# Kernel tuning notes

Measured on AMD Instinct MI355X. Metric: run time of the kernel, lower is better.

The kernel has to match this reference:

```python
import jax, jax.numpy as jnp
import numpy as np

N_NODES = 100000
N_EDGES = 1600000
NUM_GRAPHS = 128


def setup_inputs() -> dict:
    key = jax.random.key(0)
    k1, k2, k3, k4, k5, k6 = jax.random.split(key, 6)
    x = jax.random.normal(k1, (N_NODES, 69), dtype=jnp.float32)
    src = jax.random.randint(k2, (N_EDGES,), 0, N_NODES)
    dst = jax.random.randint(k3, (N_EDGES,), 0, N_NODES)
    graph_ids = jnp.sort(jax.random.randint(k4, (N_NODES,), 0, NUM_GRAPHS))
    # Glorot-uniform weights like dgl GraphConv (bias=False)
    lim1 = np.sqrt(6.0 / (69 + 128))
    lim2 = np.sqrt(6.0 / (128 + 64))
    W1 = jax.random.uniform(k5, (69, 128), minval=-lim1, maxval=lim1, dtype=jnp.float32)
    W2 = jax.random.uniform(k6, (128, 64), minval=-lim2, maxval=lim2, dtype=jnp.float32)
    return {"x": x, "W1": W1, "W2": W2, "src": src, "dst": dst, "graph_ids": graph_ids}


def _graph_conv(feat, W, src, dst, inv_sqrt_out, inv_sqrt_in, n_nodes):
    # dgl GraphConv norm='both': D_out^{-1/2} -> SpMM(A) -> D_in^{-1/2} -> W
    h = feat * inv_sqrt_out[:, None]
    agg = jax.ops.segment_sum(h[src], dst, num_segments=n_nodes)  # [N, d]
    agg = agg * inv_sqrt_in[:, None]
    return agg @ W


def reference(x, W1, W2, src, dst, graph_ids):
    n = x.shape[0]
    ones = jnp.ones((src.shape[0],), dtype=x.dtype)
    out_deg = jax.ops.segment_sum(ones, src, num_segments=n)
    in_deg = jax.ops.segment_sum(ones, dst, num_segments=n)
    inv_sqrt_out = jax.lax.rsqrt(jnp.clip(out_deg, 1.0, None))
    inv_sqrt_in = jax.lax.rsqrt(jnp.clip(in_deg, 1.0, None))

    h = _graph_conv(x, W1, src, dst, inv_sqrt_out, inv_sqrt_in, n)
    h = jax.nn.relu(h)
    h = _graph_conv(h, W2, src, dst, inv_sqrt_out, inv_sqrt_in, n)
    h = jax.nn.relu(h)
    # dgl.max_nodes: per-graph max readout -> [num_graphs, 64]
    readout = jax.ops.segment_max(h, graph_ids, num_segments=NUM_GRAPHS)
    return readout
```

## Files before the change

### kernel.cpp

```cpp
#include <hip/hip_runtime.h>

#define N_NODES 100000
#define N_EDGES 1600000
#define NUM_GRAPHS 128

#define BSH 10
#define NBUCK 98
#define NBLKP 500
#define EPB (N_EDGES / NBLKP)
#define SOFF (NBUCK * NBLKP)
#define NSCAN (2 * NBUCK * NBLKP)
#define SCAN_BS 1024
#define NBSC ((NSCAN + SCAN_BS - 1) / SCAN_BS)

__device__ __forceinline__ unsigned bf16pair(float a, float b) {
    unsigned ua = __float_as_uint(a), ub = __float_as_uint(b);
    ua = (ua + 0x7FFFu + ((ua >> 16) & 1u)) >> 16;
    ub = (ub + 0x7FFFu + ((ub >> 16) & 1u)) >> 16;
    return ua | (ub << 16);
}
__device__ __forceinline__ float bflo(unsigned u) { return __uint_as_float(u << 16); }
__device__ __forceinline__ float bfhi(unsigned u) { return __uint_as_float(u & 0xFFFF0000u); }

__global__ __launch_bounds__(256) void part_hist(const int* __restrict__ src,
                                                 const int* __restrict__ dst,
                                                 int* __restrict__ cnt) {
    __shared__ int hd[4 * NBUCK], hs[4 * NBUCK];
    int t = threadIdx.x;
    for (int i = t; i < 4 * NBUCK; i += 256) { hd[i] = 0; hs[i] = 0; }
    __syncthreads();
    int wid = t >> 6;
    int* hdw = hd + wid * NBUCK;
    int* hsw = hs + wid * NBUCK;
    int e0 = blockIdx.x * EPB;
    for (int j = 4 * t; j + 3 < EPB; j += 1024) {
        int4 s4 = *(const int4*)(src + e0 + j);
        int4 d4 = *(const int4*)(dst + e0 + j);
        atomicAdd(&hdw[d4.x >> BSH], 1); atomicAdd(&hdw[d4.y >> BSH], 1);
        atomicAdd(&hdw[d4.z >> BSH], 1); atomicAdd(&hdw[d4.w >> BSH], 1);
        atomicAdd(&hsw[s4.x >> BSH], 1); atomicAdd(&hsw[s4.y >> BSH], 1);
        atomicAdd(&hsw[s4.z >> BSH], 1); atomicAdd(&hsw[s4.w >> BSH], 1);
    }
    __syncthreads();
    int bk = blockIdx.x;
    for (int i = t; i < NBUCK; i += 256) {
        cnt[i * NBLKP + bk] = hd[i] + hd[NBUCK + i] + hd[2 * NBUCK + i] + hd[3 * NBUCK + i];
        cnt[SOFF + i * NBLKP + bk] = hs[i] + hs[NBUCK + i] + hs[2 * NBUCK + i] + hs[3 * NBUCK + i];
    }
}

__global__ __launch_bounds__(256) void scan1(const int* __restrict__ cnt, int* __restrict__ excl,
                                             int* __restrict__ blksum, int n) {
    __shared__ int tmp[256];
    int t = threadIdx.x;
    int idx0 = blockIdx.x * SCAN_BS + t * 4;
    int v[4];
#pragma unroll
    for (int k = 0; k < 4; ++k) { int i = idx0 + k; v[k] = (i < n) ? cnt[i] : 0; }
    int sum = v[0] + v[1] + v[2] + v[3];
    tmp[t] = sum;
    __syncthreads();
    for (int off = 1; off < 256; off <<= 1) {
        int y = (t >= off) ? tmp[t - off] : 0;
        __syncthreads();
        tmp[t] += y;
        __syncthreads();
    }
    int run = (t > 0) ? tmp[t - 1] : 0;
#pragma unroll
    for (int k = 0; k < 4; ++k) { int i = idx0 + k; if (i < n) excl[i] = run; run += v[k]; }
    if (t == 255) blksum[blockIdx.x] = tmp[255];
}

__global__ __launch_bounds__(256) void scan2(int* __restrict__ blksum, int nb) {
    __shared__ int tmp[256];
    int t = threadIdx.x;
    int C = (nb + 255) / 256;
    int base = t * C;
    int s = 0;
    for (int k = 0; k < C; ++k) { int i = base + k; if (i < nb) s += blksum[i]; }
    tmp[t] = s;
    __syncthreads();
    for (int off = 1; off < 256; off <<= 1) {
        int y = (t >= off) ? tmp[t - off] : 0;
        __syncthreads();
        tmp[t] += y;
        __syncthreads();
    }
    int run = (t > 0) ? tmp[t - 1] : 0;
    for (int k = 0; k < C; ++k) {
        int i = base + k;
        if (i < nb) { int v = blksum[i]; blksum[i] = run; run += v; }
    }
}

__global__ __launch_bounds__(256) void part_scatter(const int* __restrict__ src,
                                                    const int* __restrict__ dst,
                                                    const int* __restrict__ cnt,
                                                    const int* __restrict__ blk,
                                                    unsigned* __restrict__ pdst,
                                                    unsigned short* __restrict__ psrc) {
    __shared__ int cd[NBUCK], cs[NBUCK];
    int bk = blockIdx.x;
    int t = threadIdx.x;
    for (int i = t; i < NBUCK; i += 256) {
        int ii = i * NBLKP + bk;
        cd[i] = cnt[ii] + blk[ii >> 10];
        int jj = SOFF + i * NBLKP + bk;
        cs[i] = cnt[jj] + blk[jj >> 10] - N_EDGES;
    }
    __syncthreads();
    int e0 = bk * EPB;
    for (int j = 4 * t; j + 3 < EPB; j += 1024) {
        int4 s4 = *(const int4*)(src + e0 + j);
        int4 d4 = *(const int4*)(dst + e0 + j);
        int ss[4] = { s4.x, s4.y, s4.z, s4.w };
        int dd[4] = { d4.x, d4.y, d4.z, d4.w };
#pragma unroll
        for (int u = 0; u < 4; ++u) {
            int s = ss[u], d = dd[u];
            int pd = atomicAdd(&cd[d >> BSH], 1);
            pdst[pd] = (unsigned)s | ((unsigned)(d & 1023) << 17);
            int ps = atomicAdd(&cs[s >> BSH], 1);
            psrc[ps] = (unsigned short)(s & 1023);
        }
    }
}

__global__ __launch_bounds__(1024) void build_csr(const unsigned* __restrict__ pdst,
                                                  const int* __restrict__ cnt,
                                                  const int* __restrict__ blk,
                                                  int* __restrict__ ecol, int* __restrict__ row_start,
                                                  float* __restrict__ isqi, int nN) {
    __shared__ int lh[1024];
    __shared__ int lsc[1024];
    int bu = blockIdx.x;
    int i0 = bu * NBLKP;
    int b0 = cnt[i0] + blk[i0 >> 10];
    int b1;
    if (bu == NBUCK - 1) b1 = N_EDGES;
    else { int i1 = i0 + NBLKP; b1 = cnt[i1] + blk[i1 >> 10]; }
    int t = threadIdx.x;
    lh[t] = 0;
    __syncthreads();
    for (int j = b0 + t; j < b1; j += 1024)
        atomicAdd(&lh[pdst[j] >> 17], 1);
    __syncthreads();
    int myc = lh[t];
    lsc[t] = myc;
    __syncthreads();
    for (int off = 1; off < 1024; off <<= 1) {
        int y = (t >= off) ? lsc[t - off] : 0;
        __syncthreads();
        lsc[t] += y;
        __syncthreads();
    }
    int excl = lsc[t] - myc;
    int node = (bu << BSH) + t;
    if (node < nN) {
        row_start[node] = b0 + excl;
        isqi[node] = rsqrtf(fmaxf((float)myc, 1.0f));
    }
    __syncthreads();
    lh[t] = b0 + excl;
    __syncthreads();
    for (int j = b0 + t; j < b1; j += 1024) {
        unsigned w = pdst[j];
        int pos = atomicAdd(&lh[w >> 17], 1);
        ecol[pos] = (int)(w & 0x1FFFFu);
    }
}

__global__ __launch_bounds__(1024) void src_deg(const unsigned short* __restrict__ psrc,
                                                const int* __restrict__ cnt,
                                                const int* __restrict__ blk,
                                                float* __restrict__ isqo, int nN) {
    __shared__ int lh[1024];
    int bu = blockIdx.x;
    int i0 = SOFF + bu * NBLKP;
    int b0 = cnt[i0] + blk[i0 >> 10] - N_EDGES;
    int b1;
    if (bu == NBUCK - 1) b1 = N_EDGES;
    else { int i1 = i0 + NBLKP; b1 = cnt[i1] + blk[i1 >> 10] - N_EDGES; }
    int t = threadIdx.x;
    lh[t] = 0;
    __syncthreads();
    for (int j = b0 + t; j < b1; j += 1024)
        atomicAdd(&lh[psrc[j]], 1);
    __syncthreads();
    int node = (bu << BSH) + t;
    if (node < nN) isqo[node] = rsqrtf(fmaxf((float)lh[t], 1.0f));
}

__global__ void prescale_kernel(const float* __restrict__ x, const float* __restrict__ isqo,
                                unsigned* __restrict__ xsu, int nN) {
    int wave = (int)(((unsigned)blockIdx.x * blockDim.x + threadIdx.x) >> 6);
    int lane = threadIdx.x & 63;
    if (wave >= nN || lane >= 36) return;
    float s = isqo[wave];
    int c = 2 * lane;
    float a = (c < 69) ? x[(size_t)wave * 69 + c] * s : 0.0f;
    float b = (c + 1 < 69) ? x[(size_t)wave * 69 + c + 1] * s : 0.0f;
    xsu[(size_t)wave * 36 + lane] = bf16pair(a, b);
}

__global__ void gather1_kernel(const unsigned* __restrict__ feat, const int* __restrict__ ecol,
                               const int* __restrict__ row_start, const float* __restrict__ dscale,
                               float* __restrict__ agg, int nN, int nE) {
    int wave = (int)(((unsigned)blockIdx.x * blockDim.x + threadIdx.x) >> 6);
    int lane = threadIdx.x & 63;
    if (wave >= nN) return;
    int beg = row_start[wave];
    int end = (wave == nN - 1) ? nE : row_start[wave + 1];
    bool act = (lane < 36);
    float ax = 0.0f, ay = 0.0f;
    for (int j0 = beg; j0 < end; j0 += 64) {
        int ne = min(64, end - j0);
        int eidx = (lane < ne) ? ecol[j0 + lane] : 0;
        int k = 0;
        for (; k + 8 <= ne; k += 8) {
            unsigned v[8];
#pragma unroll
            for (int u = 0; u < 8; ++u) {
                int s = __shfl(eidx, k + u);
                v[u] = act ? feat[(size_t)s * 36 + lane] : 0u;
            }
#pragma unroll
            for (int u = 0; u < 8; ++u) { ax += bflo(v[u]); ay += bfhi(v[u]); }
        }
        for (; k + 2 <= ne; k += 2) {
            int s0 = __shfl(eidx, k), s1 = __shfl(eidx, k + 1);
            unsigned v0 = act ? feat[(size_t)s0 * 36 + lane] : 0u;
            unsigned v1 = act ? feat[(size_t)s1 * 36 + lane] : 0u;
            ax += bflo(v0) + bflo(v1); ay += bfhi(v0) + bfhi(v1);
        }
        for (; k < ne; ++k) {
            int s = __shfl(eidx, k);
            unsigned v = act ? feat[(size_t)s * 36 + lane] : 0u;
            ax += bflo(v); ay += bfhi(v);
        }
    }
    if (act) {
        float dsc = dscale[wave];
        ((float2*)(agg + (size_t)wave * 72))[lane] = make_float2(ax * dsc, ay * dsc);
    }
}

__global__ void gather2_kernel(const unsigned* __restrict__ feat, const int* __restrict__ ecol,
                               const int* __restrict__ row_start, const float* __restrict__ dscale,
                               float* __restrict__ agg, int nN, int nE) {
    int wave = (int)(((unsigned)blockIdx.x * blockDim.x + threadIdx.x) >> 6);
    int lane = threadIdx.x & 63;
    if (wave >= nN) return;
    int beg = row_start[wave];
    int end = (wave == nN - 1) ? nE : row_start[wave + 1];
    int half = lane >> 5;
    int c = lane & 31;
    float ax = 0.0f, ay = 0.0f;
    for (int j0 = beg; j0 < end; j0 += 64) {
        int ne = min(64, end - j0);
        int eidx = (lane < ne) ? ecol[j0 + lane] : 0;
        int k = 0;
        for (; k + 16 <= ne; k += 16) {
            unsigned v[8];
#pragma unroll
            for (int u = 0; u < 8; ++u) {
                int s = __shfl(eidx, k + 2 * u + half);
                v[u] = feat[(size_t)s * 32 + c];
            }
#pragma unroll
            for (int u = 0; u < 8; ++u) { ax += bflo(v[u]); ay += bfhi(v[u]); }
        }
        for (; k + 2 <= ne; k += 2) {
            int s = __shfl(eidx, k + half);
            unsigned v = feat[(size_t)s * 32 + c];
            ax += bflo(v); ay += bfhi(v);
        }
        if (k < ne) {
            int s = __shfl(eidx, k);
            if (half == 0) {
                unsigned v = feat[(size_t)s * 32 + c];
                ax += bflo(v); ay += bfhi(v);
            }
        }
    }
    ax += __shfl_xor(ax, 32);
    ay += __shfl_xor(ay, 32);
    if (half == 0) {
        float dsc = dscale[wave];
        ((float2*)(agg + (size_t)wave * 64))[c] = make_float2(ax * dsc, ay * dsc);
    }
}

template<int KP, int K, int NO, bool RELU, bool SCALE, bool BF16OUT>
__global__ __launch_bounds__(256) void node_gemm(const float* __restrict__ in,
                                                 const float* __restrict__ W,
                                                 const float* __restrict__ rowscale,
                                                 void* __restrict__ out, int nN) {
    constexpr int CG = NO / 8;
    constexpr int RT = 256 / CG;
    constexpr int ROWS = RT * 4;
    __shared__ float Wl[KP * NO];
    for (int i = threadIdx.x; i < KP * NO; i += 256)
        Wl[i] = (i < K * NO) ? W[i] : 0.0f;
    __syncthreads();

    int cg = threadIdx.x % CG;
    int rt = threadIdx.x / CG;
    int row0 = blockIdx.x * ROWS + rt * 4;
    int c0 = cg * 8;

    float4 accL[4] = {};
    float4 accH[4] = {};
    int rclamp[4];
#pragma unroll
    for (int r = 0; r < 4; ++r) rclamp[r] = min(row0 + r, nN - 1);

#pragma unroll 2
    for (int k4 = 0; k4 < KP / 4; ++k4) {
        float4 a[4];
#pragma unroll
        for (int r = 0; r < 4; ++r)
            a[r] = *(const float4*)(in + (size_t)rclamp[r] * KP + k4 * 4);
#pragma unroll
        for (int kk = 0; kk < 4; ++kk) {
            int k = k4 * 4 + kk;
            float4 wlo = *(const float4*)&Wl[k * NO + c0];
            float4 whi = *(const float4*)&Wl[k * NO + c0 + 4];
#pragma unroll
            for (int r = 0; r < 4; ++r) {
                float ar = (kk == 0) ? a[r].x : (kk == 1) ? a[r].y : (kk == 2) ? a[r].z : a[r].w;
                accL[r].x += ar * wlo.x; accL[r].y += ar * wlo.y;
                accL[r].z += ar * wlo.z; accL[r].w += ar * wlo.w;
                accH[r].x += ar * whi.x; accH[r].y += ar * whi.y;
                accH[r].z += ar * whi.z; accH[r].w += ar * whi.w;
            }
        }
    }

#pragma unroll
    for (int r = 0; r < 4; ++r) {
        int row = row0 + r;
        if (row < nN) {
            float4 lo = accL[r], hi = accH[r];
            if (SCALE) {
                float sc = rowscale[row];
                lo.x *= sc; lo.y *= sc; lo.z *= sc; lo.w *= sc;
                hi.x *= sc; hi.y *= sc; hi.z *= sc; hi.w *= sc;
            }
            if (RELU) {
                lo.x = fmaxf(lo.x, 0.f); lo.y = fmaxf(lo.y, 0.f);
                lo.z = fmaxf(lo.z, 0.f); lo.w = fmaxf(lo.w, 0.f);
                hi.x = fmaxf(hi.x, 0.f); hi.y = fmaxf(hi.y, 0.f);
                hi.z = fmaxf(hi.z, 0.f); hi.w = fmaxf(hi.w, 0.f);
            }
            if (BF16OUT) {
                unsigned* ob = (unsigned*)out;
                uint4 p;
                p.x = bf16pair(lo.x, lo.y); p.y = bf16pair(lo.z, lo.w);
                p.z = bf16pair(hi.x, hi.y); p.w = bf16pair(hi.z, hi.w);
                *(uint4*)(ob + (size_t)row * (NO / 2) + c0 / 2) = p;
            } else {
                float* of = (float*)out;
                *(float4*)(of + (size_t)row * NO + c0) = lo;
                *(float4*)(of + (size_t)row * NO + c0 + 4) = hi;
            }
        }
    }
}

__global__ void readout_kernel(const float* __restrict__ agg2, const int* __restrict__ gid,
                               unsigned* __restrict__ out, int nN) {
    const int NPW = 32;
    int wave = (int)(((unsigned)blockIdx.x * blockDim.x + threadIdx.x) >> 6);
    int lane = threadIdx.x & 63;
    int n0 = wave * NPW;
    if (n0 >= nN) return;
    int curg = gid[n0];
    float best = 0.0f;
    for (int i = 0; i < NPW; ++i) {
        int n = n0 + i;
        if (n >= nN) break;
        int g = gid[n];
        float v = fmaxf(agg2[(size_t)n * 64 + lane], 0.0f);
        if (g != curg) {
            atomicMax(&out[curg * 64 + lane], __float_as_uint(best));
            curg = g;
            best = v;
        } else {
            best = fmaxf(best, v);
        }
    }
    atomicMax(&out[curg * 64 + lane], __float_as_uint(best));
}

extern "C" void kernel_launch(void* const* d_in, const int* in_sizes, int n_in,
                              void* d_out, int out_size, void* d_ws, size_t ws_size,
                              hipStream_t stream) {
    const float* x   = (const float*)d_in[0];
    const float* W1  = (const float*)d_in[1];
    const float* W2  = (const float*)d_in[2];
    const int*   src = (const int*)d_in[3];
    const int*   dst = (const int*)d_in[4];
    const int*   gid = (const int*)d_in[5];

    char* w = (char*)d_ws;
    float* isqo    = (float*)w;                 w += N_NODES * 4;
    float* isqi    = (float*)w;                 w += N_NODES * 4;
    int* row_start = (int*)w;                   w += N_NODES * 4;
    int* ecol      = (int*)w;                   w += (size_t)N_EDGES * 4;
    int* cnt       = (int*)w;                   w += (size_t)NSCAN * 4;
    int* blksum    = (int*)w;                   w += 1024 * 4;
    float* bufA    = (float*)w;                 w += (size_t)N_NODES * 72 * 4;
    char* bufB     = w;
    unsigned* pdst       = (unsigned*)bufB;
    unsigned* xsu        = (unsigned*)bufB;
    unsigned short* psrc = (unsigned short*)(bufB + (size_t)N_NODES * 36 * 4);
    float* h1            = (float*)bufB;
    float* agg2          = (float*)bufB;

    hipMemsetAsync(d_out, 0, (size_t)out_size * sizeof(float), stream);

    part_hist<<<NBLKP, 256, 0, stream>>>(src, dst, cnt);
    scan1<<<NBSC, 256, 0, stream>>>(cnt, cnt, blksum, NSCAN);
    scan2<<<1, 256, 0, stream>>>(blksum, NBSC);
    part_scatter<<<NBLKP, 256, 0, stream>>>(src, dst, cnt, blksum, pdst, psrc);
    build_csr<<<NBUCK, 1024, 0, stream>>>(pdst, cnt, blksum, ecol, row_start, isqi, N_NODES);
    src_deg<<<NBUCK, 1024, 0, stream>>>(psrc, cnt, blksum, isqo, N_NODES);
    prescale_kernel<<<(N_NODES * 64 + 255) / 256, 256, 0, stream>>>(x, isqo, xsu, N_NODES);

    gather1_kernel<<<(N_NODES * 64 + 255) / 256, 256, 0, stream>>>(
        xsu, ecol, row_start, isqi, bufA, N_NODES, N_EDGES);
    node_gemm<72, 69, 128, true, false, false><<<(N_NODES + 63) / 64, 256, 0, stream>>>(
        bufA, W1, nullptr, h1, N_NODES);

    node_gemm<128, 128, 64, false, true, true><<<(N_NODES + 127) / 128, 256, 0, stream>>>(
        h1, W2, isqo, (void*)bufA, N_NODES);
    gather2_kernel<<<(N_NODES * 64 + 255) / 256, 256, 0, stream>>>(
        (const unsigned*)bufA, ecol, row_start, isqi, agg2, N_NODES, N_EDGES);

    readout_kernel<<<((N_NODES + 31) / 32 * 64 + 255) / 256, 256, 0, stream>>>(
        agg2, gid, (unsigned*)d_out, N_NODES);
}
```

Baseline: 276.9 us.

## Merge CSR/degree kernels, split gather1 rows into halves, store h1 as bf16

Three changes. First, build_csr and src_deg are fused into one launch of 2*NBUCK blocks so the two independent passes run concurrently. Second, the layer-1 features are split into a 32-word main array and a 4-word tail array, so gather1 can use both wave halves on alternate edges, as gather2 already does, instead of leaving 28 lanes idle. Third, the first GEMM writes h1 in bf16 and the second GEMM reads bf16, halving h1 traffic at some cost in precision.

```diff
diff --git a/kernel.cpp b/kernel.cpp
--- a/kernel.cpp
+++ b/kernel.cpp
@@ -127,73 +127,70 @@
     }
 }
 
-__global__ __launch_bounds__(1024) void build_csr(const unsigned* __restrict__ pdst,
-                                                  const int* __restrict__ cnt,
-                                                  const int* __restrict__ blk,
-                                                  int* __restrict__ ecol, int* __restrict__ row_start,
-                                                  float* __restrict__ isqi, int nN) {
+__global__ __launch_bounds__(1024) void phase_d(const unsigned* __restrict__ pdst,
+                                                const unsigned short* __restrict__ psrc,
+                                                const int* __restrict__ cnt,
+                                                const int* __restrict__ blk,
+                                                int* __restrict__ ecol, int* __restrict__ row_start,
+                                                float* __restrict__ isqi, float* __restrict__ isqo,
+                                                int nN) {
     __shared__ int lh[1024];
     __shared__ int lsc[1024];
-    int bu = blockIdx.x;
-    int i0 = bu * NBLKP;
-    int b0 = cnt[i0] + blk[i0 >> 10];
-    int b1;
-    if (bu == NBUCK - 1) b1 = N_EDGES;
-    else { int i1 = i0 + NBLKP; b1 = cnt[i1] + blk[i1 >> 10]; }
     int t = threadIdx.x;
-    lh[t] = 0;
-    __syncthreads();
-    for (int j = b0 + t; j < b1; j += 1024)
-        atomicAdd(&lh[pdst[j] >> 17], 1);
-    __syncthreads();
-    int myc = lh[t];
-    lsc[t] = myc;
-    __syncthreads();
-    for (int off = 1; off < 1024; off <<= 1) {
-        int y = (t >= off) ? lsc[t - off] : 0;
-        __syncthreads();
-        lsc[t] += y;
-        __syncthreads();
-    }
-    int excl = lsc[t] - myc;
-    int node = (bu << BSH) + t;
-    if (node < nN) {
-        row_start[node] = b0 + excl;
-        isqi[node] = rsqrtf(fmaxf((float)myc, 1.0f));
-    }
-    __syncthreads();
-    lh[t] = b0 + excl;
-    __syncthreads();
-    for (int j = b0 + t; j < b1; j += 1024) {
-        unsigned w = pdst[j];
-        int pos = atomicAdd(&lh[w >> 17], 1);
-        ecol[pos] = (int)(w & 0x1FFFFu);
-    }
-}
-
-__global__ __launch_bounds__(1024) void src_deg(const unsigned short* __restrict__ psrc,
-                                                const int* __restrict__ cnt,
-                                                const int* __restrict__ blk,
-                                                float* __restrict__ isqo, int nN) {
-    __shared__ int lh[1024];
-    int bu = blockIdx.x;
-    int i0 = SOFF + bu * NBLKP;
-    int b0 = cnt[i0] + blk[i0 >> 10] - N_EDGES;
-    int b1;
-    if (bu == NBUCK - 1) b1 = N_EDGES;
-    else { int i1 = i0 + NBLKP; b1 = cnt[i1] + blk[i1 >> 10] - N_EDGES; }
-    int t = threadIdx.x;
-    lh[t] = 0;
-    __syncthreads();
-    for (int j = b0 + t; j < b1; j += 1024)
-        atomicAdd(&lh[psrc[j]], 1);
-    __syncthreads();
-    int node = (bu << BSH) + t;
-    if (node < nN) isqo[node] = rsqrtf(fmaxf((float)lh[t], 1.0f));
+    if (blockIdx.x < NBUCK) {
+        int bu = blockIdx.x;
+        int i0 = bu * NBLKP;
+        int b0 = cnt[i0] + blk[i0 >> 10];
+        int b1;
+        if (bu == NBUCK - 1) b1 = N_EDGES;
+        else { int i1 = i0 + NBLKP; b1 = cnt[i1] + blk[i1 >> 10]; }
+        lh[t] = 0;
+        __syncthreads();
+        for (int j = b0 + t; j < b1; j += 1024)
+            atomicAdd(&lh[pdst[j] >> 17], 1);
+        __syncthreads();
+        int myc = lh[t];
+        lsc[t] = myc;
+        __syncthreads();
+        for (int off = 1; off < 1024; off <<= 1) {
+            int y = (t >= off) ? lsc[t - off] : 0;
+            __syncthreads();
+            lsc[t] += y;
+            __syncthreads();
+        }
+        int excl = lsc[t] - myc;
+        int node = (bu << BSH) + t;
+        if (node < nN) {
+            row_start[node] = b0 + excl;
+            isqi[node] = rsqrtf(fmaxf((float)myc, 1.0f));
+        }
+        __syncthreads();
+        lh[t] = b0 + excl;
+        __syncthreads();
+        for (int j = b0 + t; j < b1; j += 1024) {
+            unsigned w = pdst[j];
+            int pos = atomicAdd(&lh[w >> 17], 1);
+            ecol[pos] = (int)(w & 0x1FFFFu);
+        }
+    } else {
+        int bu = blockIdx.x - NBUCK;
+        int i0 = SOFF + bu * NBLKP;
+        int b0 = cnt[i0] + blk[i0 >> 10] - N_EDGES;
+        int b1;
+        if (bu == NBUCK - 1) b1 = N_EDGES;
+        else { int i1 = i0 + NBLKP; b1 = cnt[i1] + blk[i1 >> 10] - N_EDGES; }
+        lh[t] = 0;
+        __syncthreads();
+        for (int j = b0 + t; j < b1; j += 1024)
+            atomicAdd(&lh[psrc[j]], 1);
+        __syncthreads();
+        int node = (bu << BSH) + t;
+        if (node < nN) isqo[node] = rsqrtf(fmaxf((float)lh[t], 1.0f));
+    }
 }
 
 __global__ void prescale_kernel(const float* __restrict__ x, const float* __restrict__ isqo,
-                                unsigned* __restrict__ xsu, int nN) {
+                                unsigned* __restrict__ xmain, unsigned* __restrict__ xtail, int nN) {
     int wave = (int)(((unsigned)blockIdx.x * blockDim.x + threadIdx.x) >> 6);
     int lane = threadIdx.x & 63;
     if (wave >= nN || lane >= 36) return;
@@ -201,48 +198,64 @@
     int c = 2 * lane;
     float a = (c < 69) ? x[(size_t)wave * 69 + c] * s : 0.0f;
     float b = (c + 1 < 69) ? x[(size_t)wave * 69 + c + 1] * s : 0.0f;
-    xsu[(size_t)wave * 36 + lane] = bf16pair(a, b);
-}
-
-__global__ void gather1_kernel(const unsigned* __restrict__ feat, const int* __restrict__ ecol,
-                               const int* __restrict__ row_start, const float* __restrict__ dscale,
-                               float* __restrict__ agg, int nN, int nE) {
+    unsigned p = bf16pair(a, b);
+    if (lane < 32) xmain[(size_t)wave * 32 + lane] = p;
+    else           xtail[(size_t)wave * 4 + (lane - 32)] = p;
+}
+
+__global__ void gather1_kernel(const unsigned* __restrict__ xmain, const unsigned* __restrict__ xtail,
+                               const int* __restrict__ ecol, const int* __restrict__ row_start,
+                               const float* __restrict__ dscale, float* __restrict__ agg,
+                               int nN, int nE) {
     int wave = (int)(((unsigned)blockIdx.x * blockDim.x + threadIdx.x) >> 6);
     int lane = threadIdx.x & 63;
     if (wave >= nN) return;
     int beg = row_start[wave];
     int end = (wave == nN - 1) ? nE : row_start[wave + 1];
-    bool act = (lane < 36);
-    float ax = 0.0f, ay = 0.0f;
+    int half = lane >> 5;
+    int c = lane & 31;
+    bool tact = (c < 4);
+    float ax = 0.0f, ay = 0.0f, tx = 0.0f, ty = 0.0f;
     for (int j0 = beg; j0 < end; j0 += 64) {
         int ne = min(64, end - j0);
         int eidx = (lane < ne) ? ecol[j0 + lane] : 0;
         int k = 0;
-        for (; k + 8 <= ne; k += 8) {
-            unsigned v[8];
+        for (; k + 16 <= ne; k += 16) {
+            unsigned v[8], tv[8];
 #pragma unroll
             for (int u = 0; u < 8; ++u) {
-                int s = __shfl(eidx, k + u);
-                v[u] = act ? feat[(size_t)s * 36 + lane] : 0u;
-            }
-#pragma unroll
-            for (int u = 0; u < 8; ++u) { ax += bflo(v[u]); ay += bfhi(v[u]); }
+                int s = __shfl(eidx, k + 2 * u + half);
+                v[u] = xmain[(size_t)s * 32 + c];
+                tv[u] = tact ? xtail[(size_t)s * 4 + c] : 0u;
+            }
+#pragma unroll
+            for (int u = 0; u < 8; ++u) {
+                ax += bflo(v[u]); ay += bfhi(v[u]);
+                tx += bflo(tv[u]); ty += bfhi(tv[u]);
+            }
         }
         for (; k + 2 <= ne; k += 2) {
-            int s0 = __shfl(eidx, k), s1 = __shfl(eidx, k + 1);
-            unsigned v0 = act ? feat[(size_t)s0 * 36 + lane] : 0u;
-            unsigned v1 = act ? feat[(size_t)s1 * 36 + lane] : 0u;
-            ax += bflo(v0) + bflo(v1); ay += bfhi(v0) + bfhi(v1);
-        }
-        for (; k < ne; ++k) {
+            int s = __shfl(eidx, k + half);
+            unsigned v = xmain[(size_t)s * 32 + c];
+            ax += bflo(v); ay += bfhi(v);
+            if (tact) { unsigned tv = xtail[(size_t)s * 4 + c]; tx += bflo(tv); ty += bfhi(tv); }
+        }
+        if (k < ne) {
             int s = __shfl(eidx, k);
-            unsigned v = act ? feat[(size_t)s * 36 + lane] : 0u;
-            ax += bflo(v); ay += bfhi(v);
-        }
-    }
-    if (act) {
+            if (half == 0) {
+                unsigned v = xmain[(size_t)s * 32 + c];
+                ax += bflo(v); ay += bfhi(v);
+                if (tact) { unsigned tv = xtail[(size_t)s * 4 + c]; tx += bflo(tv); ty += bfhi(tv); }
+            }
+        }
+    }
+    ax += __shfl_xor(ax, 32); ay += __shfl_xor(ay, 32);
+    tx += __shfl_xor(tx, 32); ty += __shfl_xor(ty, 32);
+    if (half == 0) {
         float dsc = dscale[wave];
-        ((float2*)(agg + (size_t)wave * 72))[lane] = make_float2(ax * dsc, ay * dsc);
+        ((float2*)(agg + (size_t)wave * 72))[c] = make_float2(ax * dsc, ay * dsc);
+        if (tact)
+            ((float2*)(agg + (size_t)wave * 72 + 64))[c] = make_float2(tx * dsc, ty * dsc);
     }
 }
 
@@ -292,8 +305,8 @@
     }
 }
 
-template<int KP, int K, int NO, bool RELU, bool SCALE, bool BF16OUT>
-__global__ __launch_bounds__(256) void node_gemm(const float* __restrict__ in,
+template<int KP, int K, int NO, bool RELU, bool SCALE, bool BF16OUT, bool BF16IN>
+__global__ __launch_bounds__(256) void node_gemm(const void* __restrict__ in,
                                                  const float* __restrict__ W,
                                                  const float* __restrict__ rowscale,
                                                  void* __restrict__ out, int nN) {
@@ -316,24 +329,51 @@
 #pragma unroll
     for (int r = 0; r < 4; ++r) rclamp[r] = min(row0 + r, nN - 1);
 
+    if (BF16IN) {
+        const unsigned* inu = (const unsigned*)in;
 #pragma unroll 2
-    for (int k4 = 0; k4 < KP / 4; ++k4) {
-        float4 a[4];
-#pragma unroll
-        for (int r = 0; r < 4; ++r)
-            a[r] = *(const float4*)(in + (size_t)rclamp[r] * KP + k4 * 4);
-#pragma unroll
-        for (int kk = 0; kk < 4; ++kk) {
-            int k = k4 * 4 + kk;
-            float4 wlo = *(const float4*)&Wl[k * NO + c0];
-            float4 whi = *(const float4*)&Wl[k * NO + c0 + 4];
-#pragma unroll
-            for (int r = 0; r < 4; ++r) {
-                float ar = (kk == 0) ? a[r].x : (kk == 1) ? a[r].y : (kk == 2) ? a[r].z : a[r].w;
-                accL[r].x += ar * wlo.x; accL[r].y += ar * wlo.y;
-                accL[r].z += ar * wlo.z; accL[r].w += ar * wlo.w;
-                accH[r].x += ar * whi.x; accH[r].y += ar * whi.y;
-                accH[r].z += ar * whi.z; accH[r].w += ar * whi.w;
+        for (int k8 = 0; k8 < KP / 8; ++k8) {
+            uint4 a4[4];
+#pragma unroll
+            for (int r = 0; r < 4; ++r)
+                a4[r] = *(const uint4*)(inu + (size_t)rclamp[r] * (KP / 2) + k8 * 4);
+#pragma unroll
+            for (int kk = 0; kk < 8; ++kk) {
+                int k = k8 * 8 + kk;
+                float4 wlo = *(const float4*)&Wl[k * NO + c0];
+                float4 whi = *(const float4*)&Wl[k * NO + c0 + 4];
+#pragma unroll
+                for (int r = 0; r < 4; ++r) {
+                    unsigned wd = ((const unsigned*)&a4[r])[kk >> 1];
+                    float ar = (kk & 1) ? bfhi(wd) : bflo(wd);
+                    accL[r].x += ar * wlo.x; accL[r].y += ar * wlo.y;
+                    accL[r].z += ar * wlo.z; accL[r].w += ar * wlo.w;
+                    accH[r].x += ar * whi.x; accH[r].y += ar * whi.y;
+                    accH[r].z += ar * whi.z; accH[r].w += ar * whi.w;
+                }
+            }
+        }
+    } else {
+        const float* inf = (const float*)in;
+#pragma unroll 2
+        for (int k4 = 0; k4 < KP / 4; ++k4) {
+            float4 a[4];
+#pragma unroll
+            for (int r = 0; r < 4; ++r)
+                a[r] = *(const float4*)(inf + (size_t)rclamp[r] * KP + k4 * 4);
+#pragma unroll
+            for (int kk = 0; kk < 4; ++kk) {
+                int k = k4 * 4 + kk;
+                float4 wlo = *(const float4*)&Wl[k * NO + c0];
+                float4 whi = *(const float4*)&Wl[k * NO + c0 + 4];
+#pragma unroll
+                for (int r = 0; r < 4; ++r) {
+                    float ar = (kk == 0) ? a[r].x : (kk == 1) ? a[r].y : (kk == 2) ? a[r].z : a[r].w;
+                    accL[r].x += ar * wlo.x; accL[r].y += ar * wlo.y;
+                    accL[r].z += ar * wlo.z; accL[r].w += ar * wlo.w;
+                    accH[r].x += ar * whi.x; accH[r].y += ar * whi.y;
+                    accH[r].z += ar * whi.z; accH[r].w += ar * whi.w;
+                }
             }
         }
     }
@@ -414,9 +454,10 @@
     float* bufA    = (float*)w;                 w += (size_t)N_NODES * 72 * 4;
     char* bufB     = w;
     unsigned* pdst       = (unsigned*)bufB;
-    unsigned* xsu        = (unsigned*)bufB;
+    unsigned* xmain      = (unsigned*)bufB;
+    unsigned* xtail      = (unsigned*)(bufB + (size_t)N_NODES * 32 * 4);
     unsigned short* psrc = (unsigned short*)(bufB + (size_t)N_NODES * 36 * 4);
-    float* h1            = (float*)bufB;
+    unsigned* h1         = (unsigned*)bufB;
     float* agg2          = (float*)bufB;
 
     hipMemsetAsync(d_out, 0, (size_t)out_size * sizeof(float), stream);
@@ -425,17 +466,17 @@
     scan1<<<NBSC, 256, 0, stream>>>(cnt, cnt, blksum, NSCAN);
     scan2<<<1, 256, 0, stream>>>(blksum, NBSC);
     part_scatter<<<NBLKP, 256, 0, stream>>>(src, dst, cnt, blksum, pdst, psrc);
-    build_csr<<<NBUCK, 1024, 0, stream>>>(pdst, cnt, blksum, ecol, row_start, isqi, N_NODES);
-    src_deg<<<NBUCK, 1024, 0, stream>>>(psrc, cnt, blksum, isqo, N_NODES);
-    prescale_kernel<<<(N_NODES * 64 + 255) / 256, 256, 0, stream>>>(x, isqo, xsu, N_NODES);
+    phase_d<<<2 * NBUCK, 1024, 0, stream>>>(pdst, psrc, cnt, blksum, ecol, row_start,
+                                            isqi, isqo, N_NODES);
+    prescale_kernel<<<(N_NODES * 64 + 255) / 256, 256, 0, stream>>>(x, isqo, xmain, xtail, N_NODES);
 
     gather1_kernel<<<(N_NODES * 64 + 255) / 256, 256, 0, stream>>>(
-        xsu, ecol, row_start, isqi, bufA, N_NODES, N_EDGES);
-    node_gemm<72, 69, 128, true, false, false><<<(N_NODES + 63) / 64, 256, 0, stream>>>(
-        bufA, W1, nullptr, h1, N_NODES);
-
-    node_gemm<128, 128, 64, false, true, true><<<(N_NODES + 127) / 128, 256, 0, stream>>>(
-        h1, W2, isqo, (void*)bufA, N_NODES);
+        xmain, xtail, ecol, row_start, isqi, bufA, N_NODES, N_EDGES);
+    node_gemm<72, 69, 128, true, false, true, false><<<(N_NODES + 63) / 64, 256, 0, stream>>>(
+        (const void*)bufA, W1, nullptr, (void*)h1, N_NODES);
+
+    node_gemm<128, 128, 64, false, true, true, true><<<(N_NODES + 127) / 128, 256, 0, stream>>>(
+        (const void*)h1, W2, isqo, (void*)bufA, N_NODES);
     gather2_kernel<<<(N_NODES * 64 + 255) / 256, 256, 0, stream>>>(
         (const unsigned*)bufA, ecol, row_start, isqi, agg2, N_NODES, N_EDGES);
 
```

Result: no change. 277.6 us (+0.2%).
